# Kernel tuning notes

Measured on AMD Instinct MI355X. Metric: run time of the kernel, lower is better.

Reference implementation:

```python
import jax, jax.numpy as jnp
import numpy as np

N = 4096      # num utterances (graph nodes)
D = 512       # utt_embed_size * 2
W = 10        # att_window_size
S = 8         # num speakers
WIN = 2 * W + 1


def setup_inputs() -> dict:
    key = jax.random.key(0)
    ks = jax.random.split(key, 7)
    s = 0.05  # keep activations in a sane range through two layers
    return {
        "context_embeds": jax.random.normal(ks[0], (N, D), jnp.float32),
        "speakers": jax.random.randint(ks[1], (N,), 0, S),
        "w_gc1": jax.random.normal(ks[2], (4, D, D), jnp.float32) * s,
        "w_gc2": jax.random.normal(ks[3], (4, D, D), jnp.float32) * s,
        "w_att": jax.random.normal(ks[4], (D, D), jnp.float32) * s,
        "w_aggr1": jax.random.normal(ks[5], (D, D), jnp.float32) * s,
        "w_aggr2": jax.random.normal(ks[6], (D, D), jnp.float32) * s,
    }


def _relation_adjs(x, speakers, w_att):
    """Windowed edge attention + 4 relation-masked adjacency matrices."""
    n = x.shape[0]
    pad = jnp.zeros((W, D), x.dtype)
    padded = jnp.concatenate([pad, x, pad], axis=0)          # [n+2W, D]
    # banded gather: row j sees padded[j : j+2W+1]  == cols j-W .. j+W
    gidx = jnp.arange(n)[:, None] + jnp.arange(WIN)[None, :]
    fat = padded[gidx]
    raw = jnp.einsum('nwd,ed->nwe', fat, w_att)               # Linear: x @ W^T
    scores = jnp.einsum('nwe,ne->nw', raw, x)
    attn = jax.nn.softmax(scores, axis=1)                     # softmax over full window (pads included, as original)
    # scatter attention into a banded [n, n] mask
    cols = jnp.arange(n)[:, None] + jnp.arange(WIN)[None, :] - W
    valid = (cols >= 0) & (cols < n)
    rows = jnp.broadcast_to(jnp.arange(n)[:, None], cols.shape)
    attn_mask = jnp.zeros((n, n), x.dtype).at[
        rows, jnp.clip(cols, 0, n - 1)].add(jnp.where(valid, attn, 0.0))
    i = jnp.arange(n)[:, None]
    j = jnp.arange(n)[None, :]
    band = jnp.abs(j - i) <= W
    same_spk = speakers[:, None] == speakers[None, :]
    pred = ((j >= i) & band).astype(x.dtype) * attn_mask      # successors-in-time kept (triu) within window
    suc = ((j < i) & band).astype(x.dtype) * attn_mask        # strict past within window
    same = (same_spk & band).astype(x.dtype) * attn_mask
    diff = ((~same_spk) & band).astype(x.dtype) * attn_mask
    return jnp.stack([pred, suc, same, diff])                 # [4, n, n]


def _gcn_layer(h, adjs, w_gc, w_aggr):
    # sum_r  A_r @ (h @ W_r)  + h @ W_aggr, then relu
    hw = jnp.einsum('md,rde->rme', h, w_gc)                   # [4, n, D]
    agg = jnp.einsum('rnm,rme->ne', adjs, hw)                 # [n, D]
    return jax.nn.relu(agg + h @ w_aggr)


def reference(context_embeds, speakers, w_gc1, w_gc2, w_att, w_aggr1, w_aggr2):
    adjs = _relation_adjs(context_embeds, speakers, w_att)
    h1 = _gcn_layer(context_embeds, adjs, w_gc1, w_aggr1)
    h2 = _gcn_layer(h1, adjs, w_gc2, w_aggr2)
    return h2
```

## Files before the change

kernel.cpp:

```cpp
#include <hip/hip_runtime.h>


#define NN 4096

typedef __bf16 bf16x8 __attribute__((ext_vector_type(8)));
typedef float f32x4 __attribute__((ext_vector_type(4)));
typedef unsigned short u16;
typedef unsigned int u32;

__device__ __forceinline__ u16 f2bf(float f) {
  unsigned u = __float_as_uint(f);
  unsigned r = u + 0x7FFFu + ((u >> 16) & 1u);
  return (u16)(r >> 16);
}
__device__ __forceinline__ float bf2f(u16 h) {
  return __uint_as_float(((unsigned)h) << 16);
}
__device__ __forceinline__ float blo(u32 v) { return __uint_as_float(v << 16); }
__device__ __forceinline__ float bhi(u32 v) { return __uint_as_float(v & 0xffff0000u); }
__device__ __forceinline__ u32 packbf(float a, float b) {
  return (u32)f2bf(a) | ((u32)f2bf(b) << 16);
}

__device__ __forceinline__ void gload_lds16(const u16* g, u16* l) {
  __builtin_amdgcn_global_load_lds(
      (const __attribute__((address_space(1))) void*)g,
      (__attribute__((address_space(3))) void*)l, 16, 0, 0);
}

__global__ void prep_all(const float* __restrict__ x, const float* __restrict__ w_att,
                         const float* __restrict__ w_gc1, const float* __restrict__ w_aggr1,
                         const float* __restrict__ w_gc2, const float* __restrict__ w_aggr2,
                         const int* __restrict__ spk,
                         u16* __restrict__ Aatt, u16* __restrict__ Batt,
                         u16* __restrict__ Wt1, u16* __restrict__ Wt2,
                         float* __restrict__ xp, u32* __restrict__ xWg,
                         u32* __restrict__ h1Wg, int* __restrict__ spkp) {
  const int b = blockIdx.x, tid = threadIdx.x;
  if (b < 8192) {
    int s = b >> 3;
    int r = 512 * (b & 7) + (s >> 1);
    int c = ((s & 1) << 8) + tid;
    float v = x[(size_t)r * 512 + c];
    u16 hi = f2bf(v), lo = f2bf(v - bf2f(hi));
    u16* row = Aatt + (size_t)r * 1536;
    row[c] = hi; row[512 + c] = lo; row[1024 + c] = hi;
    xp[(size_t)(r + 16) * 512 + c] = v;
  } else if (b < 9216) {
    int idx = (b - 8192) * 256 + tid;
    int j = idx >> 9, e = idx & 511;
    float v = w_att[(size_t)e * 512 + j];
    u16 hi = f2bf(v), lo = f2bf(v - bf2f(hi));
    u16* row = Batt + (size_t)j * 1536;
    row[e] = hi; row[512 + e] = hi; row[1024 + e] = lo;
  } else if (b < 17408) {
    int lay = (b >= 13312);
    int idx = (b - (lay ? 13312 : 9216)) * 256 + tid;
    const float* g = lay ? w_gc2 : w_gc1;
    const float* wa = lay ? w_aggr2 : w_aggr1;
    u16* Wt = lay ? Wt2 : Wt1;
    int j = idx >> 9, k = idx & 511;
    int p = j >> 9, jj = j & 511;
    size_t o = (size_t)k * 512 + jj;
    float v;
    if (p == 0)      v = g[o] - g[262144 + o];
    else if (p == 1) v = g[524288 + o] - g[786432 + o];
    else if (p == 2) v = g[262144 + o] + g[786432 + o];
    else             v = wa[o];
    Wt[(size_t)j * 512 + k] = f2bf(v);
  } else if (b < 17472) {
    int idx = (b - 17408) * 256 + tid;
    int g = idx >> 9, c = idx & 511;
    int row = (g < 16) ? g : 4112 + (g - 16);
    xp[(size_t)row * 512 + c] = 0.f;
  } else if (b < 17600) {
    int idx = (b - 17472) * 256 + tid;
    int g = idx >> 10, c = idx & 1023;
    int row = (g < 16) ? g : 4112 + (g - 16);
    xWg[(size_t)row * 1024 + c] = 0;
  } else if (b < 17728) {
    int idx = (b - 17600) * 256 + tid;
    int g = idx >> 10, c = idx & 1023;
    int row = (g < 16) ? g : 4112 + (g - 16);
    h1Wg[(size_t)row * 1024 + c] = 0;
  } else {
    int idx = (b - 17728) * 256 + tid;
    if (idx < 4128)
      spkp[idx] = (idx >= 16 && idx < 4112) ? spk[idx - 16] : -9;
  }
}

__device__ __forceinline__ void xcd_align(int gx, int& bx, int& by) {
  int lid = by * gx + bx;
  int xcd = lid & 7;
  int s = lid >> 3;
  int q = s / gx;
  bx = s - q * gx;
  by = xcd * 4 + q;
}

__device__ __forceinline__ void gemm_core(const u16* __restrict__ A, const u16* __restrict__ Bt,
                                          int K, int lda, int ldb, size_t bm, size_t bn,
                                          u16 (&As)[2][8192], u16 (&Bs)[2][8192],
                                          f32x4 (&acc)[4][4]) {
  const int tid = threadIdx.x;
  const int lane = tid & 63;
  const int wave = tid >> 6;
  const int wr = wave >> 1, wc = wave & 1;
  const int arow = wr * 64 + (lane & 15);
  const int bcol = wc * 64 + (lane & 15);
  const int nt = K >> 6;

  auto STAGE = [&](int t, int bi) {
    const int k0 = t << 6;
#pragma unroll
    for (int c4 = 0; c4 < 4; ++c4) {
      const int o = (c4 * 256 + tid) * 16;
      const int r = o >> 7;
      const int sc = (((o >> 4) & 7) ^ (r & 7)) << 3;
      gload_lds16(A + (bm + r) * lda + k0 + sc, &As[bi][o >> 1]);
      gload_lds16(Bt + (bn + r) * ldb + k0 + sc, &Bs[bi][o >> 1]);
    }
  };

  STAGE(0, 0);
  for (int t = 0; t < nt; ++t) {
    const int cur = t & 1;
    if (t + 1 < nt) {
      STAGE(t + 1, cur ^ 1);
      asm volatile("s_waitcnt vmcnt(8)" ::: "memory");
    } else {
      asm volatile("s_waitcnt vmcnt(0)" ::: "memory");
    }
    __builtin_amdgcn_s_barrier();
    asm volatile("" ::: "memory");
    bf16x8 af[4][2], bfr[4][2];
#pragma unroll
    for (int i = 0; i < 4; ++i)
#pragma unroll
      for (int ks = 0; ks < 2; ++ks) {
        const int ar = arow + i * 16;
        const int ac = ((ks * 4 + (lane >> 4)) ^ (ar & 7)) << 4;
        af[i][ks] = *(const bf16x8*)((const char*)&As[cur][0] + ar * 128 + ac);
        const int br = bcol + i * 16;
        const int bc = ((ks * 4 + (lane >> 4)) ^ (br & 7)) << 4;
        bfr[i][ks] = *(const bf16x8*)((const char*)&Bs[cur][0] + br * 128 + bc);
      }
#pragma unroll
    for (int ks = 0; ks < 2; ++ks)
#pragma unroll
      for (int i = 0; i < 4; ++i)
#pragma unroll
        for (int j = 0; j < 4; ++j)
          acc[i][j] = __builtin_amdgcn_mfma_f32_16x16x32_bf16(af[i][ks], bfr[j][ks],
                                                              acc[i][j], 0, 0, 0);
    asm volatile("s_waitcnt lgkmcnt(0)" ::: "memory");
    __builtin_amdgcn_sched_barrier(0);
    __builtin_amdgcn_s_barrier();
  }
}

__global__ __launch_bounds__(256, 2) void fat_gemm(const u16* __restrict__ Aatt,
                                                   const u16* __restrict__ Wt1,
                                                   const u16* __restrict__ Batt,
                                                   u16* __restrict__ xW, float* __restrict__ y) {
  __shared__ u16 As[2][8192];
  __shared__ u16 Bs[2][8192];
  f32x4 acc[4][4] = {};
  const int tid = threadIdx.x;
  const int lane = tid & 63;
  const int wave = tid >> 6;
  const int wr = wave >> 1, wc = wave & 1;
  int bx = blockIdx.x, by = blockIdx.y;
  xcd_align(20, bx, by);
  const size_t bm = (size_t)by * 128;
  const bool yp = bx < 4;
  const size_t bn = yp ? (size_t)bx * 128 : (size_t)(bx - 4) * 128;

  if (yp)
    gemm_core(Aatt, Batt, 1536, 1536, 1536, bm, bn, As, Bs, acc);
  else
    gemm_core(Aatt, Wt1, 512, 1536, 512, bm, bn, As, Bs, acc);

  const size_t crow = bm + wr * 64 + ((lane >> 4) * 4);
  const size_t ccol = bn + wc * 64 + (lane & 15);
#pragma unroll
  for (int i = 0; i < 4; ++i)
#pragma unroll
    for (int j = 0; j < 4; ++j)
#pragma unroll
      for (int b = 0; b < 4; ++b) {
        size_t r = crow + i * 16 + b, c = ccol + j * 16;
        if (yp)
          y[r * 512 + c] = acc[i][j][b];
        else
          xW[r * 2048 + c] = f2bf(acc[i][j][b]);
      }
}

__global__ __launch_bounds__(256, 2) void gemm_l2(const u16* __restrict__ h1,
                                                  const u16* __restrict__ Wt2,
                                                  u16* __restrict__ h1W) {
  __shared__ u16 As[2][8192];
  __shared__ u16 Bs[2][8192];
  f32x4 acc[4][4] = {};
  const int tid = threadIdx.x;
  const int lane = tid & 63;
  const int wave = tid >> 6;
  const int wr = wave >> 1, wc = wave & 1;
  int bx = blockIdx.x, by = blockIdx.y;
  xcd_align(16, bx, by);
  const size_t bm = (size_t)by * 128;
  const size_t bn = (size_t)bx * 128;
  gemm_core(h1, Wt2, 512, 512, 512, bm, bn, As, Bs, acc);
  const size_t crow = bm + wr * 64 + ((lane >> 4) * 4);
  const size_t ccol = bn + wc * 64 + (lane & 15);
#pragma unroll
  for (int i = 0; i < 4; ++i)
#pragma unroll
    for (int j = 0; j < 4; ++j)
#pragma unroll
      for (int b = 0; b < 4; ++b) {
        size_t r = crow + i * 16 + b, c = ccol + j * 16;
        h1W[r * 2048 + c] = f2bf(acc[i][j][b]);
      }
}

__device__ __forceinline__ int xcd_row(int b) { return (b & 7) * 512 + (b >> 3); }

__global__ void gather1(const float* __restrict__ xp, const float* __restrict__ y,
                        const u16* __restrict__ xW, const int* __restrict__ spkp,
                        float* __restrict__ attn, u16* __restrict__ h1) {
  const int n = xcd_row(blockIdx.x);
  const int tid = threadIdx.x;
  __shared__ float ys[512];
  __shared__ float sc[21];
  __shared__ float av[21], apv[21], asv[21];
  __shared__ int sps[21];
  const int mysp = spkp[16 + n];
  ys[tid] = y[(size_t)n * 512 + tid];
  ys[tid + 256] = y[(size_t)n * 512 + tid + 256];
  if (tid < 21) sps[tid] = spkp[16 + n - 10 + tid];
  __syncthreads();
  const int wave = tid >> 6, lane = tid & 63;
  for (int w = wave; w < 21; w += 4) {
    const float* xm = xp + (size_t)(n + 6 + w) * 512;
    float p = 0.f;
#pragma unroll
    for (int i = 0; i < 8; ++i) p += xm[lane + i * 64] * ys[lane + i * 64];
#pragma unroll
    for (int off = 32; off; off >>= 1) p += __shfl_xor(p, off, 64);
    if (lane == 0) sc[w] = p;
  }
  __syncthreads();
  if (tid < 64) {
    float v = (tid < 21) ? sc[tid] : -1e30f;
    float mx = v;
#pragma unroll
    for (int off = 32; off; off >>= 1) mx = fmaxf(mx, __shfl_xor(mx, off, 64));
    float e = (tid < 21) ? __expf(v - mx) : 0.f;
    float sum = e;
#pragma unroll
    for (int off = 32; off; off >>= 1) sum += __shfl_xor(sum, off, 64);
    if (tid < 21) {
      int m = n + tid - 10;
      float a = (0 <= m && m < NN) ? (e / sum) : 0.f;
      av[tid] = a;
      apv[tid] = (tid >= 10) ? a : 0.f;
      asv[tid] = (sps[tid] == mysp) ? a : 0.f;
      attn[(size_t)n * 24 + tid] = a;
    }
  }
  __syncthreads();
  const u32* xW32 = (const u32*)xW;
  u32 hv = xW32[(size_t)n * 1024 + 768 + tid];
  float a0 = blo(hv), a1 = bhi(hv);
#pragma unroll
  for (int w = 0; w < 10; ++w) {
    const u32* row = xW32 + (ptrdiff_t)(n - 10 + w) * 1024 + tid;
    u32 vs = row[256], va = row[512];
    float s2 = asv[w], a = av[w];
    a0 += s2 * blo(vs) + a * blo(va);
    a1 += s2 * bhi(vs) + a * bhi(va);
  }
#pragma unroll
  for (int w = 10; w < 21; ++w) {
    const u32* row = xW32 + (ptrdiff_t)(n - 10 + w) * 1024 + tid;
    u32 vp = row[0], vs = row[256], va = row[512];
    float ap = apv[w], s2 = asv[w], a = av[w];
    a0 += ap * blo(vp) + s2 * blo(vs) + a * blo(va);
    a1 += ap * bhi(vp) + s2 * bhi(vs) + a * bhi(va);
  }
  ((u32*)(h1 + (size_t)n * 512))[tid] = packbf(fmaxf(a0, 0.f), fmaxf(a1, 0.f));
}

__global__ void gather2(const u16* __restrict__ h1W, const float* __restrict__ attn,
                        const int* __restrict__ spkp, float* __restrict__ out) {
  const int n = xcd_row(blockIdx.x);
  const int tid = threadIdx.x;
  __shared__ float av[21], apv[21], asv[21];
  if (tid < 21) {
    float a = attn[(size_t)n * 24 + tid];
    int sp = spkp[16 + n - 10 + tid];
    av[tid] = a;
    apv[tid] = (tid >= 10) ? a : 0.f;
    asv[tid] = (sp == spkp[16 + n]) ? a : 0.f;
  }
  __syncthreads();
  const u32* hW32 = (const u32*)h1W;
  u32 hv = hW32[(size_t)n * 1024 + 768 + tid];
  float a0 = blo(hv), a1 = bhi(hv);
#pragma unroll
  for (int w = 0; w < 10; ++w) {
    const u32* row = hW32 + (ptrdiff_t)(n - 10 + w) * 1024 + tid;
    u32 vs = row[256], va = row[512];
    float s2 = asv[w], a = av[w];
    a0 += s2 * blo(vs) + a * blo(va);
    a1 += s2 * bhi(vs) + a * bhi(va);
  }
#pragma unroll
  for (int w = 10; w < 21; ++w) {
    const u32* row = hW32 + (ptrdiff_t)(n - 10 + w) * 1024 + tid;
    u32 vp = row[0], vs = row[256], va = row[512];
    float ap = apv[w], s2 = asv[w], a = av[w];
    a0 += ap * blo(vp) + s2 * blo(vs) + a * blo(va);
    a1 += ap * bhi(vp) + s2 * bhi(vs) + a * bhi(va);
  }
  float* o = out + (size_t)n * 512 + tid * 2;
  o[0] = fmaxf(a0, 0.f);
  o[1] = fmaxf(a1, 0.f);
}

extern "C" void kernel_launch(void* const* d_in, const int* in_sizes, int n_in,
                              void* d_out, int out_size, void* d_ws, size_t ws_size,
                              hipStream_t stream) {
  const float* x = (const float*)d_in[0];
  const int* spk = (const int*)d_in[1];
  const float* w_gc1 = (const float*)d_in[2];
  const float* w_gc2 = (const float*)d_in[3];
  const float* w_att = (const float*)d_in[4];
  const float* w_aggr1 = (const float*)d_in[5];
  const float* w_aggr2 = (const float*)d_in[6];

  char* p = (char*)d_ws;
  u16* Aatt = (u16*)p;  p += (size_t)NN * 1536 * 2;
  u16* Batt = (u16*)p;  p += (size_t)512 * 1536 * 2;
  u16* Wt1 = (u16*)p;   p += (size_t)2048 * 512 * 2;
  u16* Wt2 = (u16*)p;   p += (size_t)2048 * 512 * 2;
  float* xp = (float*)p; p += (size_t)4128 * 512 * 4;
  float* y = (float*)p; p += (size_t)NN * 512 * 4;
  float* attn = (float*)p; p += (size_t)NN * 24 * 4;
  u16* xWg = (u16*)p;   p += (size_t)4128 * 2048 * 2;
  u16* h1 = (u16*)p;    p += (size_t)NN * 512 * 2;
  u16* h1Wg = (u16*)p;  p += (size_t)4128 * 2048 * 2;
  int* spkp = (int*)p;  p += (size_t)4128 * 4;

  u16* xW = xWg + (size_t)16 * 2048;
  u16* h1W = h1Wg + (size_t)16 * 2048;

  prep_all<<<17745, 256, 0, stream>>>(x, w_att, w_gc1, w_aggr1, w_gc2, w_aggr2, spk,
                                      Aatt, Batt, Wt1, Wt2, xp, (u32*)xWg, (u32*)h1Wg,
                                      spkp);

  fat_gemm<<<dim3(20, 32), 256, 0, stream>>>(Aatt, Wt1, Batt, xW, y);

  gather1<<<NN, 256, 0, stream>>>(xp, y, xW, spkp, attn, h1);

  gemm_l2<<<dim3(16, 32), 256, 0, stream>>>(h1, Wt2, h1W);

  gather2<<<NN, 256, 0, stream>>>(h1W, attn, spkp, (float*)d_out);
}
```

Measured before the change: 99.19 us.

## Split-K the attention GEMM, tile-transpose weight prep, split prep kernels

```diff
diff --git a/kernel.cpp b/kernel.cpp
--- a/kernel.cpp
+++ b/kernel.cpp
@@ -28,65 +28,103 @@
       (__attribute__((address_space(3))) void*)l, 16, 0, 0);
 }
 
-__global__ void prep_all(const float* __restrict__ x, const float* __restrict__ w_att,
-                         const float* __restrict__ w_gc1, const float* __restrict__ w_aggr1,
-                         const float* __restrict__ w_gc2, const float* __restrict__ w_aggr2,
-                         const int* __restrict__ spk,
-                         u16* __restrict__ Aatt, u16* __restrict__ Batt,
-                         u16* __restrict__ Wt1, u16* __restrict__ Wt2,
-                         float* __restrict__ xp, u32* __restrict__ xWg,
-                         u32* __restrict__ h1Wg, int* __restrict__ spkp) {
+__global__ __launch_bounds__(256) void prep_t(const float* __restrict__ w_att,
+                                              const float* __restrict__ w_gc1,
+                                              const float* __restrict__ w_aggr1,
+                                              const float* __restrict__ w_gc2,
+                                              const float* __restrict__ w_aggr2,
+                                              u16* __restrict__ Batt,
+                                              u16* __restrict__ Wt1, u16* __restrict__ Wt2) {
+  __shared__ float t[64][65];
   const int b = blockIdx.x, tid = threadIdx.x;
-  if (b < 8192) {
-    int s = b >> 3;
-    int r = 512 * (b & 7) + (s >> 1);
-    int c = ((s & 1) << 8) + tid;
-    float v = x[(size_t)r * 512 + c];
-    u16 hi = f2bf(v), lo = f2bf(v - bf2f(hi));
-    u16* row = Aatt + (size_t)r * 1536;
-    row[c] = hi; row[512 + c] = lo; row[1024 + c] = hi;
-    xp[(size_t)(r + 16) * 512 + c] = v;
-  } else if (b < 9216) {
-    int idx = (b - 8192) * 256 + tid;
-    int j = idx >> 9, e = idx & 511;
-    float v = w_att[(size_t)e * 512 + j];
-    u16 hi = f2bf(v), lo = f2bf(v - bf2f(hi));
-    u16* row = Batt + (size_t)j * 1536;
-    row[e] = hi; row[512 + e] = hi; row[1024 + e] = lo;
-  } else if (b < 17408) {
-    int lay = (b >= 13312);
-    int idx = (b - (lay ? 13312 : 9216)) * 256 + tid;
+  const int r = tid >> 6, c = tid & 63;
+  if (b < 512) {
+    const int lay = b >> 8, tb = b & 255;
+    const int jt = tb >> 3, kt = tb & 7;
     const float* g = lay ? w_gc2 : w_gc1;
     const float* wa = lay ? w_aggr2 : w_aggr1;
     u16* Wt = lay ? Wt2 : Wt1;
-    int j = idx >> 9, k = idx & 511;
-    int p = j >> 9, jj = j & 511;
-    size_t o = (size_t)k * 512 + jj;
-    float v;
-    if (p == 0)      v = g[o] - g[262144 + o];
-    else if (p == 1) v = g[524288 + o] - g[786432 + o];
-    else if (p == 2) v = g[262144 + o] + g[786432 + o];
-    else             v = wa[o];
-    Wt[(size_t)j * 512 + k] = f2bf(v);
-  } else if (b < 17472) {
-    int idx = (b - 17408) * 256 + tid;
-    int g = idx >> 9, c = idx & 511;
-    int row = (g < 16) ? g : 4112 + (g - 16);
-    xp[(size_t)row * 512 + c] = 0.f;
-  } else if (b < 17600) {
-    int idx = (b - 17472) * 256 + tid;
-    int g = idx >> 10, c = idx & 1023;
-    int row = (g < 16) ? g : 4112 + (g - 16);
-    xWg[(size_t)row * 1024 + c] = 0;
-  } else if (b < 17728) {
-    int idx = (b - 17600) * 256 + tid;
-    int g = idx >> 10, c = idx & 1023;
-    int row = (g < 16) ? g : 4112 + (g - 16);
-    h1Wg[(size_t)row * 1024 + c] = 0;
+    const int p = (jt * 64) >> 9;
+    const int jj0 = (jt * 64) & 511;
+    const int k0 = kt * 64;
+#pragma unroll
+    for (int i = 0; i < 16; ++i) {
+      int rr = r + i * 4;
+      size_t o = (size_t)(k0 + rr) * 512 + jj0 + c;
+      float v;
+      if (p == 0)      v = g[o] - g[262144 + o];
+      else if (p == 1) v = g[524288 + o] - g[786432 + o];
+      else if (p == 2) v = g[262144 + o] + g[786432 + o];
+      else             v = wa[o];
+      t[c][rr] = v;
+    }
+    __syncthreads();
+#pragma unroll
+    for (int i = 0; i < 16; ++i) {
+      int jl = r + i * 4;
+      Wt[(size_t)(jt * 64 + jl) * 512 + k0 + c] = f2bf(t[jl][c]);
+    }
   } else {
-    int idx = (b - 17728) * 256 + tid;
-    if (idx < 4128)
-      spkp[idx] = (idx >= 16 && idx < 4112) ? spk[idx - 16] : -9;
+    const int tb = b - 512;
+    const int et = tb >> 3, jt2 = tb & 7;
+    const int e0 = et * 64, j0 = jt2 * 64;
+#pragma unroll
+    for (int i = 0; i < 16; ++i) {
+      int rr = r + i * 4;
+      t[c][rr] = w_att[(size_t)(e0 + rr) * 512 + j0 + c];
+    }
+    __syncthreads();
+#pragma unroll
+    for (int i = 0; i < 16; ++i) {
+      int jl = r + i * 4;
+      float v = t[jl][c];
+      u16 hi = f2bf(v), lo = f2bf(v - bf2f(hi));
+      u16* row = Batt + (size_t)(j0 + jl) * 1536;
+      row[e0 + c] = hi;
+      row[512 + e0 + c] = hi;
+      row[1024 + e0 + c] = lo;
+    }
+  }
+}
+
+__global__ __launch_bounds__(256) void prep_main(const float* __restrict__ x,
+                                                 const int* __restrict__ spk,
+                                                 u16* __restrict__ Aatt,
+                                                 float* __restrict__ xp,
+                                                 u32* __restrict__ xWg,
+                                                 u32* __restrict__ h1Wg,
+                                                 int* __restrict__ spkp) {
+  const int tid = threadIdx.x;
+  for (int vb = blockIdx.x; vb < 8529; vb += 2048) {
+    if (vb < 8192) {
+      int s = vb >> 3;
+      int r = 512 * (vb & 7) + (s >> 1);
+      int c = ((s & 1) << 8) + tid;
+      float v = x[(size_t)r * 512 + c];
+      u16 hi = f2bf(v), lo = f2bf(v - bf2f(hi));
+      u16* row = Aatt + (size_t)r * 1536;
+      row[c] = hi; row[512 + c] = lo; row[1024 + c] = hi;
+      xp[(size_t)(r + 16) * 512 + c] = v;
+    } else if (vb < 8256) {
+      int idx = (vb - 8192) * 256 + tid;
+      int g = idx >> 9, c = idx & 511;
+      int row = (g < 16) ? g : 4112 + (g - 16);
+      xp[(size_t)row * 512 + c] = 0.f;
+    } else if (vb < 8384) {
+      int idx = (vb - 8256) * 256 + tid;
+      int g = idx >> 10, c = idx & 1023;
+      int row = (g < 16) ? g : 4112 + (g - 16);
+      xWg[(size_t)row * 1024 + c] = 0;
+    } else if (vb < 8512) {
+      int idx = (vb - 8384) * 256 + tid;
+      int g = idx >> 10, c = idx & 1023;
+      int row = (g < 16) ? g : 4112 + (g - 16);
+      h1Wg[(size_t)row * 1024 + c] = 0;
+    } else {
+      int idx = (vb - 8512) * 256 + tid;
+      if (idx < 4128)
+        spkp[idx] = (idx >= 16 && idx < 4112) ? spk[idx - 16] : -9;
+    }
   }
 }
 
@@ -172,18 +210,20 @@
   const int wave = tid >> 6;
   const int wr = wave >> 1, wc = wave & 1;
   int bx = blockIdx.x, by = blockIdx.y;
-  xcd_align(20, bx, by);
+  xcd_align(28, bx, by);
   const size_t bm = (size_t)by * 128;
-  const bool yp = bx < 4;
-  const size_t bn = yp ? (size_t)bx * 128 : (size_t)(bx - 4) * 128;
+  const bool yp = bx < 12;
+  const int kp = yp ? (bx >> 2) : 0;
+  const size_t bn = yp ? (size_t)(bx & 3) * 128 : (size_t)(bx - 12) * 128;
 
   if (yp)
-    gemm_core(Aatt, Batt, 1536, 1536, 1536, bm, bn, As, Bs, acc);
+    gemm_core(Aatt + kp * 512, Batt + kp * 512, 512, 1536, 1536, bm, bn, As, Bs, acc);
   else
     gemm_core(Aatt, Wt1, 512, 1536, 512, bm, bn, As, Bs, acc);
 
   const size_t crow = bm + wr * 64 + ((lane >> 4) * 4);
   const size_t ccol = bn + wc * 64 + (lane & 15);
+  float* yk = y + (size_t)kp * NN * 512;
 #pragma unroll
   for (int i = 0; i < 4; ++i)
 #pragma unroll
@@ -192,7 +232,7 @@
       for (int b = 0; b < 4; ++b) {
         size_t r = crow + i * 16 + b, c = ccol + j * 16;
         if (yp)
-          y[r * 512 + c] = acc[i][j][b];
+          yk[r * 512 + c] = acc[i][j][b];
         else
           xW[r * 2048 + c] = f2bf(acc[i][j][b]);
       }
@@ -238,8 +278,13 @@
   __shared__ float av[21], apv[21], asv[21];
   __shared__ int sps[21];
   const int mysp = spkp[16 + n];
-  ys[tid] = y[(size_t)n * 512 + tid];
-  ys[tid + 256] = y[(size_t)n * 512 + tid + 256];
+  {
+    const float* y0 = y + (size_t)n * 512;
+    const float* y1 = y0 + (size_t)NN * 512;
+    const float* y2 = y1 + (size_t)NN * 512;
+    ys[tid] = y0[tid] + y1[tid] + y2[tid];
+    ys[tid + 256] = y0[tid + 256] + y1[tid + 256] + y2[tid + 256];
+  }
   if (tid < 21) sps[tid] = spkp[16 + n - 10 + tid];
   __syncthreads();
   const int wave = tid >> 6, lane = tid & 63;
@@ -348,7 +393,7 @@
   u16* Wt1 = (u16*)p;   p += (size_t)2048 * 512 * 2;
   u16* Wt2 = (u16*)p;   p += (size_t)2048 * 512 * 2;
   float* xp = (float*)p; p += (size_t)4128 * 512 * 4;
-  float* y = (float*)p; p += (size_t)NN * 512 * 4;
+  float* y = (float*)p; p += (size_t)3 * NN * 512 * 4;
   float* attn = (float*)p; p += (size_t)NN * 24 * 4;
   u16* xWg = (u16*)p;   p += (size_t)4128 * 2048 * 2;
   u16* h1 = (u16*)p;    p += (size_t)NN * 512 * 2;
@@ -358,11 +403,11 @@
   u16* xW = xWg + (size_t)16 * 2048;
   u16* h1W = h1Wg + (size_t)16 * 2048;
 
-  prep_all<<<17745, 256, 0, stream>>>(x, w_att, w_gc1, w_aggr1, w_gc2, w_aggr2, spk,
-                                      Aatt, Batt, Wt1, Wt2, xp, (u32*)xWg, (u32*)h1Wg,
-                                      spkp);
-
-  fat_gemm<<<dim3(20, 32), 256, 0, stream>>>(Aatt, Wt1, Batt, xW, y);
+  prep_t<<<576, 256, 0, stream>>>(w_att, w_gc1, w_aggr1, w_gc2, w_aggr2, Batt, Wt1, Wt2);
+
+  prep_main<<<2048, 256, 0, stream>>>(x, spk, Aatt, xp, (u32*)xWg, (u32*)h1Wg, spkp);
+
+  fat_gemm<<<dim3(28, 32), 256, 0, stream>>>(Aatt, Wt1, Batt, xW, y);
 
   gather1<<<NN, 256, 0, stream>>>(xp, y, xW, spkp, attn, h1);
 
```

Result: faster. 91.88 us (-7.4%).
